# Kernel tuning notes

Measured on AMD Instinct MI355X. Metric: run time of the kernel, lower is better.

The kernel has to match this reference:

```python
import jax, jax.numpy as jnp
import numpy as np

B, S, H, A, E = 64, 1024, 1024, 512, 512


def setup_inputs() -> dict:
    key = jax.random.key(0)
    ks = jax.random.split(key, 13)
    sc = 0.02
    return {
        "inputs": jax.random.normal(ks[0], (B, E), jnp.float32),
        "states": jax.random.normal(ks[1], (B, H), jnp.float32),
        "encoded": jax.random.normal(ks[2], (B, S, H), jnp.float32),
        "W_enc": jax.random.normal(ks[3], (H, A), jnp.float32) * sc,
        "b_enc": jax.random.normal(ks[4], (A,), jnp.float32) * sc,
        "W_dec": jax.random.normal(ks[5], (H, A), jnp.float32) * sc,
        "b_dec": jax.random.normal(ks[6], (A,), jnp.float32) * sc,
        "w_out": jax.random.normal(ks[7], (A,), jnp.float32) * sc,
        "b_out": jax.random.normal(ks[8], (1,), jnp.float32) * sc,
        "W_ih": jax.random.normal(ks[9], (E + H, 3 * H), jnp.float32) * sc,
        "b_ih": jax.random.normal(ks[10], (3 * H,), jnp.float32) * sc,
        "W_hh": jax.random.normal(ks[11], (H, 3 * H), jnp.float32) * sc,
        "b_hh": jax.random.normal(ks[12], (3 * H,), jnp.float32) * sc,
    }


def reference(inputs, states, encoded, W_enc, b_enc, W_dec, b_dec, w_out, b_out,
              W_ih, b_ih, W_hh, b_hh):
    # setup_memory: project encoder states once  [B,S,H] @ [H,A] -> [B,S,A]
    enc_proj = jnp.einsum('bsh,ha->bsa', encoded, W_enc) + b_enc
    # Bahdanau additive attention
    dec_proj = states @ W_dec + b_dec                       # [B,A]
    scores = jnp.einsum('bsa,a->bs', jnp.tanh(enc_proj + dec_proj[:, None, :]), w_out) + b_out[0]
    weights = jax.nn.softmax(scores, axis=1)                # [B,S]
    attention = jnp.einsum('bs,bsh->bh', weights, encoded)  # [B,H]
    x = jnp.concatenate([inputs, attention], axis=-1)       # [B,E+H]
    # GRUCell (PyTorch gate order r, z, n)
    gi = x @ W_ih + b_ih                                    # [B,3H]
    gh = states @ W_hh + b_hh                               # [B,3H]
    i_r, i_z, i_n = jnp.split(gi, 3, axis=-1)
    h_r, h_z, h_n = jnp.split(gh, 3, axis=-1)
    r = jax.nn.sigmoid(i_r + h_r)
    z = jax.nn.sigmoid(i_z + h_z)
    n = jnp.tanh(i_n + r * h_n)
    h_new = (1.0 - z) * n + z * states
    return h_new
```

## Files before the change

kernel.cpp:

```cpp
#include <hip/hip_runtime.h>
#include <hip/hip_bf16.h>


typedef __attribute__((ext_vector_type(8))) __bf16 bf16x8;
typedef __attribute__((ext_vector_type(4))) __bf16 bf16x4;
typedef __attribute__((ext_vector_type(4))) float f32x4;

__device__ __forceinline__ float fast_tanh(float x) {
  float xa = fminf(fmaxf(x, -15.f), 15.f);
  float e = __expf(2.f * xa);
  return (e - 1.f) / (e + 1.f);
}

__global__ __launch_bounds__(256) void wenc_t_kernel(const float* __restrict__ W,
                                                     __bf16* __restrict__ Wt) {
  __shared__ float tile[32][33];
  int k0 = blockIdx.x * 32, a0 = blockIdx.y * 32;
  int tid = threadIdx.x;
  int r = tid >> 3, c4 = (tid & 7) * 4;
  f32x4 v = *(const f32x4*)(W + (long)(k0 + r) * 512 + a0 + c4);
  tile[r][c4 + 0] = v.x; tile[r][c4 + 1] = v.y;
  tile[r][c4 + 2] = v.z; tile[r][c4 + 3] = v.w;
  __syncthreads();
  int a = tid >> 3, k4 = (tid & 7) * 4;
  bf16x4 o = { (__bf16)tile[k4 + 0][a], (__bf16)tile[k4 + 1][a],
               (__bf16)tile[k4 + 2][a], (__bf16)tile[k4 + 3][a] };
  *(bf16x4*)(Wt + (long)(a0 + a) * 1024 + k0 + k4) = o;
}

__global__ __launch_bounds__(256) void dec_proj_kernel(
    const float* __restrict__ states, const float* __restrict__ W_dec,
    const float* __restrict__ b_enc, const float* __restrict__ b_dec,
    float* __restrict__ addv) {
  int b = blockIdx.x, tid = threadIdx.x;
  int a = blockIdx.y * 256 + tid;
  __shared__ float sl[1024];
  for (int i = tid; i < 1024; i += 256) sl[i] = states[b * 1024 + i];
  __syncthreads();
  float c0 = 0.f, c1 = 0.f, c2 = 0.f, c3 = 0.f;
#pragma unroll 4
  for (int i = 0; i < 256; ++i) {
    c0 += sl[i]         * W_dec[(i)        * 512 + a];
    c1 += sl[i + 256]   * W_dec[(i + 256)  * 512 + a];
    c2 += sl[i + 512]   * W_dec[(i + 512)  * 512 + a];
    c3 += sl[i + 768]   * W_dec[(i + 768)  * 512 + a];
  }
  addv[b * 512 + a] = c0 + c1 + c2 + c3 + b_enc[a] + b_dec[a];
}

__global__ __launch_bounds__(512, 4) void enc_score_kernel(
    const float* __restrict__ encoded,
    const __bf16* __restrict__ Wt,
    const float* __restrict__ addv,
    const float* __restrict__ w_out,
    float* __restrict__ psc)
{
  __shared__ __attribute__((aligned(16))) char bsm[65536 + 1024];
  float* red = (float*)(bsm + 65536);

  const int d = blockIdx.x;
  const int xcd = d & 7;
  const int slot = d >> 3;
  const int bn = slot & 3;
  const int bm = ((slot >> 2) << 3) | xcd;

  const int tid = threadIdx.x;
  const int lane = tid & 63;
  const int wid = tid >> 6;
  const int lr = lane & 15;
  const int lkb = lane >> 4;

  const long row0 = (long)bm * 256;
  const int col0 = bn * 128;

  const float* pa0 = encoded + (row0 + wid * 32 + lr) * 1024 + lkb * 8;
  const float* pa1 = pa0 + 16 * 1024;

  const int scol = tid >> 2;
  const int skq = tid & 3;
  const __bf16* wtb = Wt + (long)(col0 + scol) * 1024 + skq * 64;
  const int ssw = (scol & 31) << 4;

  const int rswE = lr << 4;
  const int rswO = (lr << 4) | 256;
  const int bB = lr * 512;

  f32x4 acc[2][8];
#pragma unroll
  for (int m = 0; m < 2; ++m)
#pragma unroll
    for (int n = 0; n < 8; ++n) acc[m][n] = (f32x4){0.f, 0.f, 0.f, 0.f};

  for (int ck = 0; ck < 4; ++ck) {
    if (ck) __syncthreads();
#pragma unroll
    for (int j = 0; j < 8; ++j) {
      bf16x8 v = *(const bf16x8*)(wtb + ck * 256 + j * 8);
      *(bf16x8*)(bsm + scol * 512 + ((skq * 128 + j * 16) ^ ssw)) = v;
    }
    __syncthreads();

#pragma unroll
    for (int ktc = 0; ktc < 8; ++ktc) {
      const int kt = ck * 8 + ktc;
      f32x4 x0 = *(const f32x4*)(pa0 + kt * 32);
      f32x4 x1 = *(const f32x4*)(pa0 + kt * 32 + 4);
      f32x4 y0 = *(const f32x4*)(pa1 + kt * 32);
      f32x4 y1 = *(const f32x4*)(pa1 + kt * 32 + 4);
      bf16x8 a0, a1;
#pragma unroll
      for (int i = 0; i < 4; ++i) {
        a0[i] = (__bf16)x0[i]; a0[4 + i] = (__bf16)x1[i];
        a1[i] = (__bf16)y0[i]; a1[4 + i] = (__bf16)y1[i];
      }
      const int kbase = (ktc << 6) | (lkb << 4);
      const int offE = kbase ^ rswE;
      const int offO = kbase ^ rswO;
      __builtin_amdgcn_s_setprio(1);
#pragma unroll
      for (int n = 0; n < 8; ++n) {
        bf16x8 bf_ = *(const bf16x8*)(bsm + bB + n * 8192 + ((n & 1) ? offO : offE));
        acc[0][n] = __builtin_amdgcn_mfma_f32_16x16x32_bf16(a0, bf_, acc[0][n], 0, 0, 0);
        acc[1][n] = __builtin_amdgcn_mfma_f32_16x16x32_bf16(a1, bf_, acc[1][n], 0, 0, 0);
      }
      __builtin_amdgcn_s_setprio(0);
    }
  }

  const int b = bm >> 2;
  const float* addvb = addv + b * 512;
  float rowsum[2][4];
#pragma unroll
  for (int m = 0; m < 2; ++m)
#pragma unroll
    for (int reg = 0; reg < 4; ++reg) rowsum[m][reg] = 0.f;

#pragma unroll
  for (int n = 0; n < 8; ++n) {
    int col = col0 + n * 16 + lr;
    float av = addvb[col];
    float wo = w_out[col];
#pragma unroll
    for (int m = 0; m < 2; ++m)
#pragma unroll
      for (int reg = 0; reg < 4; ++reg)
        rowsum[m][reg] += fast_tanh(acc[m][n][reg] + av) * wo;
  }
#pragma unroll
  for (int m = 0; m < 2; ++m)
#pragma unroll
    for (int reg = 0; reg < 4; ++reg) {
      float v = rowsum[m][reg];
      v += __shfl_xor(v, 1, 64);
      v += __shfl_xor(v, 2, 64);
      v += __shfl_xor(v, 4, 64);
      v += __shfl_xor(v, 8, 64);
      rowsum[m][reg] = v;
    }
  __syncthreads();
  if (lr == 0) {
#pragma unroll
    for (int m = 0; m < 2; ++m)
#pragma unroll
      for (int reg = 0; reg < 4; ++reg)
        red[wid * 32 + m * 16 + lkb * 4 + reg] = rowsum[m][reg];
  }
  __syncthreads();
  if (tid < 256)
    psc[(long)bn * 65536 + row0 + tid] = red[tid];
}

__global__ __launch_bounds__(256) void softmax_kernel(const float* __restrict__ psc,
                                                      float* __restrict__ wts) {
  int b = blockIdx.x, tid = threadIdx.x;
  __shared__ float sred[8];
  float sc[4];
  float mx = -1e30f;
#pragma unroll
  for (int i = 0; i < 4; ++i) {
    long r = (long)b * 1024 + tid + i * 256;
    sc[i] = psc[r] + psc[65536 + r] + psc[2 * 65536 + r] + psc[3 * 65536 + r];
    mx = fmaxf(mx, sc[i]);
  }
  for (int off = 1; off < 64; off <<= 1) mx = fmaxf(mx, __shfl_xor(mx, off, 64));
  if ((tid & 63) == 0) sred[tid >> 6] = mx;
  __syncthreads();
  mx = fmaxf(fmaxf(sred[0], sred[1]), fmaxf(sred[2], sred[3]));
  float e[4], sum = 0.f;
#pragma unroll
  for (int i = 0; i < 4; ++i) {
    e[i] = __expf(sc[i] - mx);
    sum += e[i];
  }
  for (int off = 1; off < 64; off <<= 1) sum += __shfl_xor(sum, off, 64);
  if ((tid & 63) == 0) sred[4 + (tid >> 6)] = sum;
  __syncthreads();
  sum = sred[4] + sred[5] + sred[6] + sred[7];
  float inv = 1.f / sum;
#pragma unroll
  for (int i = 0; i < 4; ++i) wts[(long)b * 1024 + tid + i * 256] = e[i] * inv;
}

__global__ __launch_bounds__(256) void att_part_kernel(const float* __restrict__ encoded,
                                                       const float* __restrict__ wts,
                                                       float* __restrict__ attp) {
  int chunk = blockIdx.x;
  int b = blockIdx.y;
  int tid = threadIdx.x;
  f32x4 a0 = (f32x4){0.f, 0.f, 0.f, 0.f};
  f32x4 a1 = a0, a2 = a0, a3 = a0;
  const float* base = encoded + ((long)b * 1024 + chunk * 64) * 1024 + tid * 4;
  const float* w = wts + b * 1024 + chunk * 64;
#pragma unroll 4
  for (int s = 0; s < 64; s += 4) {
    f32x4 v0 = *(const f32x4*)(base + (long)(s + 0) * 1024);
    f32x4 v1 = *(const f32x4*)(base + (long)(s + 1) * 1024);
    f32x4 v2 = *(const f32x4*)(base + (long)(s + 2) * 1024);
    f32x4 v3 = *(const f32x4*)(base + (long)(s + 3) * 1024);
    a0 += v0 * w[s]; a1 += v1 * w[s + 1]; a2 += v2 * w[s + 2]; a3 += v3 * w[s + 3];
  }
  *(f32x4*)(attp + ((long)(b * 16 + chunk)) * 1024 + tid * 4) = (a0 + a1) + (a2 + a3);
}

__global__ __launch_bounds__(256) void xcat_kernel(const float* __restrict__ inputs,
                                                   const float* __restrict__ attp,
                                                   float* __restrict__ xcat) {
  int b = blockIdx.y;
  int k = blockIdx.x * 256 + threadIdx.x;
  float v;
  if (k < 512) {
    v = inputs[b * 512 + k];
  } else {
    int h = k - 512;
    v = 0.f;
#pragma unroll
    for (int c = 0; c < 16; ++c) v += attp[((long)(b * 16 + c)) * 1024 + h];
  }
  xcat[(long)b * 1536 + k] = v;
}

__global__ __launch_bounds__(512) void gru_gemv_kernel(
    const float* __restrict__ xcat, const float* __restrict__ states,
    const float* __restrict__ W_ih, const float* __restrict__ b_ih,
    const float* __restrict__ W_hh, const float* __restrict__ b_hh,
    float* __restrict__ gi, float* __restrict__ gh) {
  __shared__ float sx[12288];
  const int dd = blockIdx.x;
  const int xcd = dd & 7;
  const int n = dd >> 3;
  const int cgrp = xcd + 8 * (n >> 3);
  const int bg = n & 7;
  const int tid = threadIdx.x;
  const int lcol = tid & 255;
  const int bsel = (tid >> 8) * 4;

  if (cgrp < 12) {
    const int col = cgrp * 256 + lcol;
    const float* xb = xcat + (long)bg * 8 * 1536;
    for (int i = tid; i < 3072; i += 512) ((f32x4*)sx)[i] = ((const f32x4*)xb)[i];
    __syncthreads();
    float a0 = b_ih[col], a1 = a0, a2 = a0, a3 = a0;
    const float* x0 = sx + (bsel + 0) * 1536;
    const float* x1 = sx + (bsel + 1) * 1536;
    const float* x2 = sx + (bsel + 2) * 1536;
    const float* x3 = sx + (bsel + 3) * 1536;
    for (int k = 0; k < 1536; k += 4) {
      f32x4 v0 = *(const f32x4*)(x0 + k);
      f32x4 v1 = *(const f32x4*)(x1 + k);
      f32x4 v2 = *(const f32x4*)(x2 + k);
      f32x4 v3 = *(const f32x4*)(x3 + k);
#pragma unroll
      for (int j = 0; j < 4; ++j) {
        float w = W_ih[(long)(k + j) * 3072 + col];
        a0 += v0[j] * w; a1 += v1[j] * w; a2 += v2[j] * w; a3 += v3[j] * w;
      }
    }
    long o = (long)(bg * 8 + bsel) * 3072 + col;
    gi[o] = a0; gi[o + 3072] = a1; gi[o + 6144] = a2; gi[o + 9216] = a3;
  } else {
    const int col = (cgrp - 12) * 256 + lcol;
    const float* sb = states + (long)bg * 8 * 1024;
    for (int i = tid; i < 2048; i += 512) ((f32x4*)sx)[i] = ((const f32x4*)sb)[i];
    __syncthreads();
    float a0 = b_hh[col], a1 = a0, a2 = a0, a3 = a0;
    const float* x0 = sx + (bsel + 0) * 1024;
    const float* x1 = sx + (bsel + 1) * 1024;
    const float* x2 = sx + (bsel + 2) * 1024;
    const float* x3 = sx + (bsel + 3) * 1024;
    for (int k = 0; k < 1024; k += 4) {
      f32x4 v0 = *(const f32x4*)(x0 + k);
      f32x4 v1 = *(const f32x4*)(x1 + k);
      f32x4 v2 = *(const f32x4*)(x2 + k);
      f32x4 v3 = *(const f32x4*)(x3 + k);
#pragma unroll
      for (int j = 0; j < 4; ++j) {
        float w = W_hh[(long)(k + j) * 3072 + col];
        a0 += v0[j] * w; a1 += v1[j] * w; a2 += v2[j] * w; a3 += v3[j] * w;
      }
    }
    long o = (long)(bg * 8 + bsel) * 3072 + col;
    gh[o] = a0; gh[o + 3072] = a1; gh[o + 6144] = a2; gh[o + 9216] = a3;
  }
}

__global__ __launch_bounds__(256) void gate_kernel(const float* __restrict__ gi,
                                                   const float* __restrict__ gh,
                                                   const float* __restrict__ states,
                                                   float* __restrict__ out) {
  int b = blockIdx.y;
  int j = blockIdx.x * 256 + threadIdx.x;
  long o = (long)b * 3072;
  float ir = gi[o + j], hr = gh[o + j];
  float iz = gi[o + 1024 + j], hz = gh[o + 1024 + j];
  float in_ = gi[o + 2048 + j], hn = gh[o + 2048 + j];
  float r = 1.f / (1.f + __expf(-(ir + hr)));
  float z = 1.f / (1.f + __expf(-(iz + hz)));
  float n = fast_tanh(in_ + r * hn);
  out[(long)b * 1024 + j] = (1.f - z) * n + z * states[(long)b * 1024 + j];
}

extern "C" void kernel_launch(void* const* d_in, const int* in_sizes, int n_in,
                              void* d_out, int out_size, void* d_ws, size_t ws_size,
                              hipStream_t stream) {
  const float* inputs  = (const float*)d_in[0];
  const float* states  = (const float*)d_in[1];
  const float* encoded = (const float*)d_in[2];
  const float* W_enc   = (const float*)d_in[3];
  const float* b_enc   = (const float*)d_in[4];
  const float* W_dec   = (const float*)d_in[5];
  const float* b_dec   = (const float*)d_in[6];
  const float* w_out   = (const float*)d_in[7];
  const float* W_ih    = (const float*)d_in[9];
  const float* b_ih    = (const float*)d_in[10];
  const float* W_hh    = (const float*)d_in[11];
  const float* b_hh    = (const float*)d_in[12];
  float* out = (float*)d_out;
  float* ws = (float*)d_ws;

  float* addv = ws;
  float* psc  = ws + 32768;
  float* wts  = ws + 294912;
  float* attp = ws + 360448;
  float* xcat = ws + 1409024;
  float* gi   = ws + 1507328;
  float* gh   = ws + 1703936;
  __bf16* Wt  = (__bf16*)(ws + 1900544);

  wenc_t_kernel<<<dim3(32, 16), 256, 0, stream>>>(W_enc, Wt);

  dim3 gA(64, 2);
  dec_proj_kernel<<<gA, 256, 0, stream>>>(states, W_dec, b_enc, b_dec, addv);

  enc_score_kernel<<<1024, 512, 0, stream>>>(encoded, Wt, addv, w_out, psc);

  softmax_kernel<<<64, 256, 0, stream>>>(psc, wts);

  dim3 gD(16, 64);
  att_part_kernel<<<gD, 256, 0, stream>>>(encoded, wts, attp);

  dim3 gE(6, 64);
  xcat_kernel<<<gE, 256, 0, stream>>>(inputs, attp, xcat);

  gru_gemv_kernel<<<192, 512, 0, stream>>>(xcat, states, W_ih, b_ih, W_hh, b_hh, gi, gh);

  dim3 gG(4, 64);
  gate_kernel<<<gG, 256, 0, stream>>>(gi, gh, states, out);
}
```

Before: 396.4 us.

## Double-buffer enc_score GEMM tiles via direct global-to-LDS loads with 128x128 tiles

```diff
diff --git a/kernel.cpp b/kernel.cpp
--- a/kernel.cpp
+++ b/kernel.cpp
@@ -11,6 +11,11 @@
   float e = __expf(2.f * xa);
   return (e - 1.f) / (e + 1.f);
 }
+
+#define GLOAD16(G, L)                                                              \
+  __builtin_amdgcn_global_load_lds(                                                \
+      (const __attribute__((address_space(1))) unsigned int*)(const void*)(G),     \
+      (__attribute__((address_space(3))) unsigned int*)(void*)(L), 16, 0, 0)
 
 __global__ __launch_bounds__(256) void wenc_t_kernel(const float* __restrict__ W,
                                                      __bf16* __restrict__ Wt) {
@@ -48,15 +53,15 @@
   addv[b * 512 + a] = c0 + c1 + c2 + c3 + b_enc[a] + b_dec[a];
 }
 
-__global__ __launch_bounds__(512, 4) void enc_score_kernel(
+__global__ __launch_bounds__(256, 3) void enc_score_kernel(
     const float* __restrict__ encoded,
     const __bf16* __restrict__ Wt,
     const float* __restrict__ addv,
     const float* __restrict__ w_out,
     float* __restrict__ psc)
 {
-  __shared__ __attribute__((aligned(16))) char bsm[65536 + 1024];
-  float* red = (float*)(bsm + 65536);
+  __shared__ __attribute__((aligned(16))) char smem[50176];
+  float* red = (float*)(smem + 49152);
 
   const int d = blockIdx.x;
   const int xcd = d & 7;
@@ -67,87 +72,95 @@
   const int tid = threadIdx.x;
   const int lane = tid & 63;
   const int wid = tid >> 6;
+  const int wr = wid >> 1;
+  const int wc = wid & 1;
   const int lr = lane & 15;
   const int lkb = lane >> 4;
 
-  const long row0 = (long)bm * 256;
+  const long row0 = (long)bm * 128;
   const int col0 = bn * 128;
 
-  const float* pa0 = encoded + (row0 + wid * 32 + lr) * 1024 + lkb * 8;
-  const float* pa1 = pa0 + 16 * 1024;
-
-  const int scol = tid >> 2;
-  const int skq = tid & 3;
-  const __bf16* wtb = Wt + (long)(col0 + scol) * 1024 + skq * 64;
-  const int ssw = (scol & 31) << 4;
-
-  const int rswE = lr << 4;
-  const int rswO = (lr << 4) | 256;
-  const int bB = lr * 512;
-
-  f32x4 acc[2][8];
-#pragma unroll
-  for (int m = 0; m < 2; ++m)
-#pragma unroll
-    for (int n = 0; n < 8; ++n) acc[m][n] = (f32x4){0.f, 0.f, 0.f, 0.f};
-
-  for (int ck = 0; ck < 4; ++ck) {
-    if (ck) __syncthreads();
-#pragma unroll
-    for (int j = 0; j < 8; ++j) {
-      bf16x8 v = *(const bf16x8*)(wtb + ck * 256 + j * 8);
-      *(bf16x8*)(bsm + scol * 512 + ((skq * 128 + j * 16) ^ ssw)) = v;
-    }
+  const int aslot = (tid & 7) ^ ((tid >> 3) & 7);
+  const char* gA = (const char*)encoded + (row0 + (tid >> 3)) * 4096 + (aslot << 4);
+  const int bslot = (tid & 3) ^ ((tid >> 3) & 3);
+  const char* gB = (const char*)Wt + (long)(col0 + (tid >> 2)) * 2048 + (bslot << 4);
+  const int ldsW = wid * 1024;
+
+  const int aoff0 = ((2 * lkb) ^ (lr & 7)) << 4;
+  const int aoff1 = ((2 * lkb + 1) ^ (lr & 7)) << 4;
+  const int boff = (lkb ^ ((lr >> 1) & 3)) << 4;
+  const int aRowB = (wr * 64 + lr) * 128;
+  const int bColB = (wc * 64 + lr) * 64;
+
+  f32x4 acc[4][4];
+#pragma unroll
+  for (int m = 0; m < 4; ++m)
+#pragma unroll
+    for (int n = 0; n < 4; ++n) acc[m][n] = (f32x4){0.f, 0.f, 0.f, 0.f};
+
+#define STAGE(BUF, KT) do {                                                        \
+    _Pragma("unroll") for (int _i = 0; _i < 4; ++_i)                               \
+      GLOAD16(gA + (long)_i * 131072 + (KT) * 128,                                 \
+              smem + (BUF) * 16384 + _i * 4096 + ldsW);                            \
+    _Pragma("unroll") for (int _i = 0; _i < 2; ++_i)                               \
+      GLOAD16(gB + (long)_i * 131072 + (KT) * 64,                                  \
+              smem + 32768 + (BUF) * 8192 + _i * 4096 + ldsW);                     \
+  } while (0)
+
+#define COMPUTE(BUF) do {                                                          \
+    const char* _Ab = smem + (BUF) * 16384;                                        \
+    const char* _Bb = smem + 32768 + (BUF) * 8192;                                 \
+    bf16x8 _af[4], _bv[4];                                                         \
+    _Pragma("unroll") for (int _m = 0; _m < 4; ++_m) {                             \
+      f32x4 _lo = *(const f32x4*)(_Ab + aRowB + _m * 2048 + aoff0);                \
+      f32x4 _hi = *(const f32x4*)(_Ab + aRowB + _m * 2048 + aoff1);                \
+      _Pragma("unroll") for (int _j = 0; _j < 4; ++_j) {                           \
+        _af[_m][_j] = (__bf16)_lo[_j]; _af[_m][4 + _j] = (__bf16)_hi[_j];          \
+      }                                                                            \
+    }                                                                              \
+    _Pragma("unroll") for (int _n = 0; _n < 4; ++_n)                               \
+      _bv[_n] = *(const bf16x8*)(_Bb + bColB + _n * 1024 + boff);                  \
+    _Pragma("unroll") for (int _m = 0; _m < 4; ++_m)                               \
+      _Pragma("unroll") for (int _n = 0; _n < 4; ++_n)                             \
+        acc[_m][_n] =                                                              \
+            __builtin_amdgcn_mfma_f32_16x16x32_bf16(_af[_m], _bv[_n], acc[_m][_n], 0, 0, 0); \
+  } while (0)
+
+  STAGE(0, 0);
+  __syncthreads();
+  int buf = 0;
+  for (int kt = 0; kt < 32; ++kt) {
+    if (kt < 31) STAGE(buf ^ 1, kt + 1);
+    COMPUTE(buf);
     __syncthreads();
-
-#pragma unroll
-    for (int ktc = 0; ktc < 8; ++ktc) {
-      const int kt = ck * 8 + ktc;
-      f32x4 x0 = *(const f32x4*)(pa0 + kt * 32);
-      f32x4 x1 = *(const f32x4*)(pa0 + kt * 32 + 4);
-      f32x4 y0 = *(const f32x4*)(pa1 + kt * 32);
-      f32x4 y1 = *(const f32x4*)(pa1 + kt * 32 + 4);
-      bf16x8 a0, a1;
-#pragma unroll
-      for (int i = 0; i < 4; ++i) {
-        a0[i] = (__bf16)x0[i]; a0[4 + i] = (__bf16)x1[i];
-        a1[i] = (__bf16)y0[i]; a1[4 + i] = (__bf16)y1[i];
-      }
-      const int kbase = (ktc << 6) | (lkb << 4);
-      const int offE = kbase ^ rswE;
-      const int offO = kbase ^ rswO;
-      __builtin_amdgcn_s_setprio(1);
-#pragma unroll
-      for (int n = 0; n < 8; ++n) {
-        bf16x8 bf_ = *(const bf16x8*)(bsm + bB + n * 8192 + ((n & 1) ? offO : offE));
-        acc[0][n] = __builtin_amdgcn_mfma_f32_16x16x32_bf16(a0, bf_, acc[0][n], 0, 0, 0);
-        acc[1][n] = __builtin_amdgcn_mfma_f32_16x16x32_bf16(a1, bf_, acc[1][n], 0, 0, 0);
-      }
-      __builtin_amdgcn_s_setprio(0);
-    }
-  }
-
-  const int b = bm >> 2;
+    buf ^= 1;
+  }
+
+#undef STAGE
+#undef COMPUTE
+
+  const int b = bm >> 3;
   const float* addvb = addv + b * 512;
-  float rowsum[2][4];
-#pragma unroll
-  for (int m = 0; m < 2; ++m)
+  float rowsum[4][4];
+#pragma unroll
+  for (int m = 0; m < 4; ++m)
 #pragma unroll
     for (int reg = 0; reg < 4; ++reg) rowsum[m][reg] = 0.f;
 
 #pragma unroll
-  for (int n = 0; n < 8; ++n) {
-    int col = col0 + n * 16 + lr;
-    float av = addvb[col];
-    float wo = w_out[col];
-#pragma unroll
-    for (int m = 0; m < 2; ++m)
+  for (int m = 0; m < 4; ++m) {
+#pragma unroll
+    for (int n = 0; n < 4; ++n) {
+      int col = col0 + wc * 64 + n * 16 + lr;
+      float av = addvb[col];
+      float wo = w_out[col];
 #pragma unroll
       for (int reg = 0; reg < 4; ++reg)
         rowsum[m][reg] += fast_tanh(acc[m][n][reg] + av) * wo;
-  }
-#pragma unroll
-  for (int m = 0; m < 2; ++m)
+    }
+  }
+#pragma unroll
+  for (int m = 0; m < 4; ++m)
 #pragma unroll
     for (int reg = 0; reg < 4; ++reg) {
       float v = rowsum[m][reg];
@@ -157,17 +170,16 @@
       v += __shfl_xor(v, 8, 64);
       rowsum[m][reg] = v;
     }
-  __syncthreads();
   if (lr == 0) {
 #pragma unroll
-    for (int m = 0; m < 2; ++m)
+    for (int m = 0; m < 4; ++m)
 #pragma unroll
       for (int reg = 0; reg < 4; ++reg)
-        red[wid * 32 + m * 16 + lkb * 4 + reg] = rowsum[m][reg];
-  }
-  __syncthreads();
-  if (tid < 256)
-    psc[(long)bn * 65536 + row0 + tid] = red[tid];
+        red[(wr * 64 + m * 16 + lkb * 4 + reg) * 2 + wc] = rowsum[m][reg];
+  }
+  __syncthreads();
+  if (tid < 128)
+    psc[(long)bn * 65536 + row0 + tid] = red[tid * 2] + red[tid * 2 + 1];
 }
 
 __global__ __launch_bounds__(256) void softmax_kernel(const float* __restrict__ psc,
@@ -351,7 +363,7 @@
   dim3 gA(64, 2);
   dec_proj_kernel<<<gA, 256, 0, stream>>>(states, W_dec, b_enc, b_dec, addv);
 
-  enc_score_kernel<<<1024, 512, 0, stream>>>(encoded, Wt, addv, w_out, psc);
+  enc_score_kernel<<<2048, 256, 0, stream>>>(encoded, Wt, addv, w_out, psc);
 
   softmax_kernel<<<64, 256, 0, stream>>>(psc, wts);
 
```

Result: faster. 333.6 us (-15.8%).
